# Kernel optimization log

Measured on AMD Instinct MI355X. Metric: run time of the kernel, lower is better.

Reference implementation:

```python
import jax, jax.numpy as jnp
import numpy as np

D_MODEL = 1024
D_STATE = 16
D_CONV = 4
EXPAND = 2
D_INNER = EXPAND * D_MODEL          # 2048
DT_RANK = (D_MODEL + 15) // 16      # 64
B, L = 4, 2048


def setup_inputs() -> dict:
    key = jax.random.key(0)
    ks = jax.random.split(key, 10)
    s = 0.02
    x = jax.random.normal(ks[0], (B, L, D_MODEL), dtype=jnp.float32)
    # weights stored (in, out) so y = x @ W
    W_in = jax.random.normal(ks[1], (D_MODEL, 2 * D_INNER), dtype=jnp.float32) * s
    conv_w = jax.random.normal(ks[2], (D_INNER, D_CONV), dtype=jnp.float32) * 0.2
    conv_b = jnp.zeros((D_INNER,), dtype=jnp.float32)
    W_xproj = jax.random.normal(ks[3], (D_INNER, DT_RANK + 2 * D_STATE), dtype=jnp.float32) * s
    W_dt = jax.random.normal(ks[4], (DT_RANK, D_INNER), dtype=jnp.float32) * s
    b_dt = jax.random.uniform(ks[5], (D_INNER,), dtype=jnp.float32, minval=-4.0, maxval=-2.0)
    # S4D real init: A = -exp(A_log), A_log = log(1..d_state)
    A_log = jnp.log(jnp.broadcast_to(jnp.arange(1, D_STATE + 1, dtype=jnp.float32), (D_INNER, D_STATE)))
    Dp = jnp.ones((D_INNER,), dtype=jnp.float32)
    W_out = jax.random.normal(ks[6], (D_INNER, D_MODEL), dtype=jnp.float32) * s
    return {"x": x, "W_in": W_in, "conv_w": conv_w, "conv_b": conv_b,
            "W_xproj": W_xproj, "W_dt": W_dt, "b_dt": b_dt,
            "A_log": A_log, "Dp": Dp, "W_out": W_out}


def _causal_depthwise_conv(u, conv_w, conv_b):
    # u: (B, L, D_INNER); depthwise causal conv, kernel D_CONV
    uc = jnp.transpose(u, (0, 2, 1))                      # (B, D, L)
    k = conv_w[:, None, :]                                # (D, 1, K)
    y = jax.lax.conv_general_dilated(
        uc, k, window_strides=(1,), padding=[(D_CONV - 1, 0)],
        feature_group_count=D_INNER,
        dimension_numbers=('NCH', 'OIH', 'NCH'))
    y = y + conv_b[None, :, None]
    return jnp.transpose(y, (0, 2, 1))                    # (B, L, D)


def _selective_scan(u, delta, A, Bm, Cm, Dp):
    # u, delta: (B, L, d); A: (d, n); Bm, Cm: (B, L, n)
    def step(h, inp):
        u_t, dt_t, B_t, C_t = inp                         # (B,d),(B,d),(B,n),(B,n)
        dA = jnp.exp(dt_t[..., None] * A)                 # (B, d, n)
        h = h * dA + (dt_t * u_t)[..., None] * B_t[:, None, :]
        y = jnp.einsum('bdn,bn->bd', h, C_t)
        return h, y

    h0 = jnp.zeros((u.shape[0], u.shape[2], A.shape[1]), dtype=u.dtype)
    xs = (jnp.swapaxes(u, 0, 1), jnp.swapaxes(delta, 0, 1),
          jnp.swapaxes(Bm, 0, 1), jnp.swapaxes(Cm, 0, 1))
    _, ys = jax.lax.scan(step, h0, xs)
    y = jnp.swapaxes(ys, 0, 1)                            # (B, L, d)
    return y + u * Dp


def reference(x, W_in, conv_w, conv_b, W_xproj, W_dt, b_dt, A_log, Dp, W_out):
    xz = x @ W_in                                         # (B, L, 2*D_INNER)
    u, z = jnp.split(xz, 2, axis=-1)
    u = jax.nn.silu(_causal_depthwise_conv(u, conv_w, conv_b))
    proj = u @ W_xproj                                    # (B, L, DT_RANK + 2*D_STATE)
    dt_r = proj[..., :DT_RANK]
    Bm = proj[..., DT_RANK:DT_RANK + D_STATE]
    Cm = proj[..., DT_RANK + D_STATE:]
    delta = jax.nn.softplus(dt_r @ W_dt + b_dt)           # (B, L, D_INNER)
    A = -jnp.exp(A_log)                                   # (D_INNER, D_STATE)
    y = _selective_scan(u, delta, A, Bm, Cm, Dp)
    y = y * jax.nn.silu(z)
    return y @ W_out
```

## Files before the change

### kernel.cpp

```cpp
#include <hip/hip_runtime.h>
#include <hip/hip_bf16.h>
#include <math.h>

#define MTOK   8192
#define LSEQ   2048
#define NBATCH 4
#define DMODEL 1024
#define DINNER 2048
#define DSTATE 16
#define DTRANK 64
#define NXZ    4096
#define CHUNK  64
#define NCH    32
#define NPROJ  (MTOK * 96)
#define SPLITK 4

typedef _Float16 f16;
using f16x8 = __attribute__((ext_vector_type(8))) _Float16;
using f16x4 = __attribute__((ext_vector_type(4))) _Float16;
using f32x4 = __attribute__((ext_vector_type(4))) float;

__device__ __forceinline__ float silu_f(float x) { return x / (1.f + __expf(-x)); }

__device__ __forceinline__ void gload_lds16(const void* g, void* l) {
    __builtin_amdgcn_global_load_lds(
        (const __attribute__((address_space(1))) void*)g,
        (__attribute__((address_space(3))) void*)l, 16, 0, 0);
}

__global__ __launch_bounds__(256)
void cvt_f2h(const float* __restrict__ in, f16* __restrict__ out, int n4)
{
    const int i = blockIdx.x * 256 + threadIdx.x;
    if (i >= n4) return;
    const float4 v = ((const float4*)in)[i];
    f16x4 o;
    o[0] = (f16)v.x; o[1] = (f16)v.y; o[2] = (f16)v.z; o[3] = (f16)v.w;
    ((f16x4*)out)[i] = o;
}

__global__ __launch_bounds__(256)
void tcvt(const float* __restrict__ in, f16* __restrict__ out, int R, int C)
{
    __shared__ float t[32][33];
    const int c0 = blockIdx.x * 32, r0 = blockIdx.y * 32;
    const int tx = threadIdx.x & 31, ty = threadIdx.x >> 5;
    #pragma unroll
    for (int j = 0; j < 4; ++j)
        t[ty + 8 * j][tx] = in[(size_t)(r0 + ty + 8 * j) * C + c0 + tx];
    __syncthreads();
    #pragma unroll
    for (int j = 0; j < 4; ++j)
        out[(size_t)(c0 + ty + 8 * j) * R + r0 + tx] = (f16)t[tx][ty + 8 * j];
}

__global__ __launch_bounds__(512, 1)
void hgemm256p(const f16* __restrict__ A, int lda,
               const f16* __restrict__ Bt, int ldb,
               f16* __restrict__ C, int ldc,
               int K, f16* __restrict__ C2, int splitcol)
{
    __shared__ __align__(16) f16 SA[2][16384];
    __shared__ __align__(16) f16 SB[2][16384];

    const int tid  = threadIdx.x;
    const int lane = tid & 63, w = tid >> 6;
    const int wr = w >> 2, wc = w & 3;
    const int row0 = blockIdx.x * 256;
    int col0 = blockIdx.y * 256;

    const int frow = lane & 15;
    const int nt = K / 64;

    auto issue_half = [&](int q) {
        const int t = q >> 2, j = q & 3, buf = t & 1, k0 = t * 64;
        const bool isA = (j >= 2);
        const int hh = j & 1;
        const f16* base = isA ? (A  + (size_t)(row0 + hh * 128) * lda + k0)
                              : (Bt + (size_t)(col0 + hh * 128) * ldb + k0);
        const int ld = isA ? lda : ldb;
        f16* dst = (isA ? &SA[buf][0] : &SB[buf][0]) + hh * 8192;
        #pragma unroll
        for (int r2 = 0; r2 < 2; ++r2) {
            const int ch = r2 * 512 + tid;
            const int grow  = ch >> 3;
            const int gunit = (ch & 7) ^ (grow & 7);
            gload_lds16(base + (size_t)grow * ld + gunit * 8, dst + ch * 8);
        }
    };

    int next = 0;
    for (; next < 6 && next < 4 * nt; ++next) issue_half(next);
    asm volatile("s_waitcnt vmcnt(4)" ::: "memory");
    asm volatile("s_barrier" ::: "memory");

    f32x4 acc[8][4] = {};

    for (int t = 0; t < nt; ++t) {
        const int buf = t & 1;
        const char* Ab = (const char*)&SA[buf][0];
        const char* Bb = (const char*)&SB[buf][0];
        f16x8 bf[4][2];
        #pragma unroll
        for (int p = 0; p < 4; ++p) {
            f16x8 af[2][2];
            if (p == 0) {
                #pragma unroll
                for (int n = 0; n < 4; ++n)
                    #pragma unroll
                    for (int ks = 0; ks < 2; ++ks) {
                        const int R = wc * 64 + n * 16 + frow;
                        const int off = R * 128 +
                            ((ks * 64 + (lane >> 4) * 16) ^ ((R & 7) << 4));
                        bf[n][ks] = *(const f16x8*)(Bb + off);
                    }
            }
            #pragma unroll
            for (int i = 0; i < 2; ++i)
                #pragma unroll
                for (int ks = 0; ks < 2; ++ks) {
                    const int R = wr * 128 + (2 * p + i) * 16 + frow;
                    const int off = R * 128 +
                        ((ks * 64 + (lane >> 4) * 16) ^ ((R & 7) << 4));
                    af[i][ks] = *(const f16x8*)(Ab + off);
                }
            if (next < 4 * nt) issue_half(next++);
            asm volatile("s_barrier" ::: "memory");
            asm volatile("s_waitcnt lgkmcnt(0)" ::: "memory");
            __builtin_amdgcn_sched_barrier(0);
            __builtin_amdgcn_s_setprio(1);
            #pragma unroll
            for (int i = 0; i < 2; ++i)
                #pragma unroll
                for (int n = 0; n < 4; ++n)
                    #pragma unroll
                    for (int ks = 0; ks < 2; ++ks)
                        acc[2 * p + i][n] = __builtin_amdgcn_mfma_f32_16x16x32_f16(
                            af[i][ks], bf[n][ks], acc[2 * p + i][n], 0, 0, 0);
            __builtin_amdgcn_s_setprio(0);
            if (p == 3 && t + 1 < nt) {
                if (next >= 4 * t + 10) asm volatile("s_waitcnt vmcnt(4)" ::: "memory");
                else                    asm volatile("s_waitcnt vmcnt(0)" ::: "memory");
            }
            asm volatile("s_barrier" ::: "memory");
        }
    }

    f16* Cw = C;
    if (C2 != nullptr && col0 >= splitcol) { Cw = C2; col0 -= splitcol; }

    const int rbase = row0 + wr * 128 + (lane >> 4) * 4;
    const int cbase = col0 + wc * 64 + (lane & 15);
    #pragma unroll
    for (int m = 0; m < 8; ++m) {
        #pragma unroll
        for (int n = 0; n < 4; ++n) {
            const int col = cbase + n * 16;
            #pragma unroll
            for (int r = 0; r < 4; ++r)
                Cw[(size_t)(rbase + m * 16 + r) * ldc + col] = (f16)acc[m][n][r];
        }
    }
}

template<int EPI, typename OUT_T>
__global__ __launch_bounds__(256)
void hgemm128(const f16* __restrict__ A, int lda,
              const f16* __restrict__ Bt, int ldb,
              OUT_T* __restrict__ C, int ldc,
              int K, const float* __restrict__ bias,
              OUT_T* __restrict__ C2, int splitcol)
{
    __shared__ __align__(16) f16 As[2][128 * 32];
    __shared__ __align__(16) f16 Bs[2][128 * 32];

    const int tid  = threadIdx.x;
    const int lane = tid & 63, wave = tid >> 6;
    const int wr = wave >> 1, wc = wave & 1;
    const int row0 = blockIdx.x * 128;
    int col0 = blockIdx.y * 128;

    const int lrow = lane >> 2;
    const int lcol = ((lane & 3) ^ ((lane >> 3) & 3)) * 8;
    const f16* Agw = A  + (size_t)(row0 + wave * 32 + lrow) * lda + lcol;
    const f16* Bgw = Bt + (size_t)(col0 + wave * 32 + lrow) * ldb + lcol;
    const int ldsbase = (wave * 32) * 32;

    const int frow = lane & 15;
    const int fk   = (((lane >> 4) ^ ((frow >> 1) & 3))) * 8;
    const int nt = K / 32;

    f32x4 acc[4][4] = {};

    #pragma unroll
    for (int r = 0; r < 2; ++r) {
        gload_lds16(Agw + (size_t)r * 16 * lda, &As[0][ldsbase + r * 16 * 32]);
        gload_lds16(Bgw + (size_t)r * 16 * ldb, &Bs[0][ldsbase + r * 16 * 32]);
    }

    int cur = 0;
    for (int kt = 0; kt < nt; ++kt) {
        __syncthreads();
        if (kt + 1 < nt) {
            const int k0 = (kt + 1) * 32;
            #pragma unroll
            for (int r = 0; r < 2; ++r) {
                gload_lds16(Agw + (size_t)r * 16 * lda + k0, &As[cur ^ 1][ldsbase + r * 16 * 32]);
                gload_lds16(Bgw + (size_t)r * 16 * ldb + k0, &Bs[cur ^ 1][ldsbase + r * 16 * 32]);
            }
        }
        f16x8 af[4], bf[4];
        #pragma unroll
        for (int m = 0; m < 4; ++m)
            af[m] = *(const f16x8*)&As[cur][(wr * 64 + m * 16 + frow) * 32 + fk];
        #pragma unroll
        for (int n = 0; n < 4; ++n)
            bf[n] = *(const f16x8*)&Bs[cur][(wc * 64 + n * 16 + frow) * 32 + fk];
        #pragma unroll
        for (int m = 0; m < 4; ++m)
            #pragma unroll
            for (int n = 0; n < 4; ++n)
                acc[m][n] = __builtin_amdgcn_mfma_f32_16x16x32_f16(af[m], bf[n], acc[m][n], 0, 0, 0);
        cur ^= 1;
    }

    OUT_T* Cw = C;
    if (C2 != nullptr && col0 >= splitcol) { Cw = C2; col0 -= splitcol; }

    const int rbase = row0 + wr * 64 + (lane >> 4) * 4;
    const int cbase = col0 + wc * 64 + (lane & 15);
    #pragma unroll
    for (int m = 0; m < 4; ++m) {
        #pragma unroll
        for (int n = 0; n < 4; ++n) {
            const int col = cbase + n * 16;
            #pragma unroll
            for (int r = 0; r < 4; ++r) {
                const int row = rbase + m * 16 + r;
                float tv = acc[m][n][r];
                if (EPI == 1) {
                    tv += bias[col];
                    tv = (tv > 20.f) ? tv : __logf(1.f + __expf(tv));
                }
                Cw[(size_t)row * ldc + col] = (OUT_T)tv;
            }
        }
    }
}

__global__ __launch_bounds__(256)
void hgemm_n96(const f16* __restrict__ A,
               const f16* __restrict__ Bt,
               float* __restrict__ part)
{
    __shared__ __align__(16) f16 As[128][40];
    __shared__ __align__(16) f16 Bs[96][40];

    const int tid = threadIdx.x, lane = tid & 63, wave = tid >> 6;
    const int row0 = blockIdx.x * 128;
    const int sk = blockIdx.y;
    const int kbase = sk * (DINNER / SPLITK);

    const int srow = tid >> 1, skoff = (tid & 1) * 16;
    const f16* Ag = A  + (size_t)(row0 + srow) * DINNER + kbase + skoff;
    const f16* Bg = Bt + (size_t)srow * DINNER + kbase + skoff;

    const int frow = lane & 15, fk = (lane >> 4) * 8;

    f32x4 acc[2][6] = {};

    for (int kk = 0; kk < DINNER / SPLITK; kk += 32) {
        const f16x8 a0 = *(const f16x8*)(Ag + kk);
        const f16x8 a1 = *(const f16x8*)(Ag + kk + 8);
        f16x8 b0 = {}, b1 = {};
        if (tid < 192) { b0 = *(const f16x8*)(Bg + kk); b1 = *(const f16x8*)(Bg + kk + 8); }
        __syncthreads();
        *(f16x8*)&As[srow][skoff]     = a0;
        *(f16x8*)&As[srow][skoff + 8] = a1;
        if (tid < 192) {
            *(f16x8*)&Bs[srow][skoff]     = b0;
            *(f16x8*)&Bs[srow][skoff + 8] = b1;
        }
        __syncthreads();

        f16x8 af[2], bf[6];
        #pragma unroll
        for (int m = 0; m < 2; ++m)
            af[m] = *(const f16x8*)&As[wave * 32 + m * 16 + frow][fk];
        #pragma unroll
        for (int n = 0; n < 6; ++n)
            bf[n] = *(const f16x8*)&Bs[n * 16 + frow][fk];
        #pragma unroll
        for (int m = 0; m < 2; ++m)
            #pragma unroll
            for (int n = 0; n < 6; ++n)
                acc[m][n] = __builtin_amdgcn_mfma_f32_16x16x32_f16(af[m], bf[n], acc[m][n], 0, 0, 0);
    }

    #pragma unroll
    for (int m = 0; m < 2; ++m)
        #pragma unroll
        for (int n = 0; n < 6; ++n) {
            const int col = n * 16 + (lane & 15);
            #pragma unroll
            for (int r = 0; r < 4; ++r) {
                const int row = row0 + wave * 32 + m * 16 + (lane >> 4) * 4 + r;
                part[((size_t)sk * MTOK + row) * 96 + col] = acc[m][n][r];
            }
        }
}

__global__ __launch_bounds__(256)
void reduce3(const float* __restrict__ part, float* __restrict__ proj,
             f16* __restrict__ projh)
{
    const int e = blockIdx.x * 256 + threadIdx.x;
    float s = 0.f;
    #pragma unroll
    for (int i = 0; i < SPLITK; ++i) s += part[(size_t)i * NPROJ + e];
    proj[e]  = s;
    projh[e] = (f16)s;
}

__global__ __launch_bounds__(256)
void conv_silu_kernel(const f16* __restrict__ uph,
                      const float* __restrict__ cw, const float* __restrict__ cb,
                      f16* __restrict__ uh)
{
    const int mt  = blockIdx.x;
    const int ml0 = mt * 8;
    const int l0  = ml0 & (LSEQ - 1);
    const int d   = threadIdx.x * 8;

    float w[8][4];
    #pragma unroll
    for (int c = 0; c < 8; ++c) {
        const float4 wv = *(const float4*)(cw + (size_t)(d + c) * 4);
        w[c][0] = wv.x; w[c][1] = wv.y; w[c][2] = wv.z; w[c][3] = wv.w;
    }
    float bias[8];
    {
        const float4 b0 = *(const float4*)(cb + d);
        const float4 b1 = *(const float4*)(cb + d + 4);
        bias[0] = b0.x; bias[1] = b0.y; bias[2] = b0.z; bias[3] = b0.w;
        bias[4] = b1.x; bias[5] = b1.y; bias[6] = b1.z; bias[7] = b1.w;
    }

    f16x8 r[11];
    if (l0 != 0) {
        #pragma unroll
        for (int i = 0; i < 11; ++i)
            r[i] = *(const f16x8*)(uph + (size_t)(ml0 - 3 + i) * DINNER + d);
    } else {
        r[0] = f16x8{}; r[1] = f16x8{}; r[2] = f16x8{};
        #pragma unroll
        for (int i = 3; i < 11; ++i)
            r[i] = *(const f16x8*)(uph + (size_t)(ml0 - 3 + i) * DINNER + d);
    }

    #pragma unroll
    for (int i = 0; i < 8; ++i) {
        f16x8 o;
        #pragma unroll
        for (int c = 0; c < 8; ++c) {
            float a = bias[c];
            #pragma unroll
            for (int j = 0; j < 4; ++j)
                a = fmaf((float)r[i + j][c], w[c][j], a);
            o[c] = (f16)silu_f(a);
        }
        *(f16x8*)(uh + (size_t)(ml0 + i) * DINNER + d) = o;
    }
}

__device__ __forceinline__ bool load_A(const float* __restrict__ A_log, int d,
                                       float* Av)
{
    #pragma unroll
    for (int n = 0; n < DSTATE; ++n)
        Av[n] = -__expf(A_log[(size_t)d * DSTATE + n]);
    bool p = true;
    #pragma unroll
    for (int n = 1; n < DSTATE; ++n) {
        const float r = Av[n] / Av[0];
        if (fabsf(r - (float)(n + 1)) > 1e-3f) p = false;
    }
    return p;
}

__global__ __launch_bounds__(256)
void scan_pass1(const f16* __restrict__ uh,
                const f16* __restrict__ deltah,
                const float* __restrict__ proj,
                const float* __restrict__ A_log,
                f16* __restrict__ Sbufh, float* __restrict__ sumdt)
{
    const int d = blockIdx.x * 256 + threadIdx.x;
    const int c = blockIdx.y;
    const int b = blockIdx.z;

    float Av[DSTATE];
    const bool pw = load_A(A_log, d, Av);
    const float Av0 = Av[0];

    const float* projb = proj + ((size_t)b * LSEQ + (size_t)c * CHUNK) * 96 + 64;

    float S[DSTATE];
    #pragma unroll
    for (int n = 0; n < DSTATE; ++n) S[n] = 0.f;
    float sdt = 0.f;

    const size_t tok0 = (size_t)b * LSEQ + (size_t)c * CHUNK;
    if (pw) {
        for (int l = 0; l < CHUNK; ++l) {
            const float* pr = projb + (size_t)l * 96;
            const float dt = (float)deltah[(tok0 + l) * DINNER + d];
            const float uu = (float)uh[(tok0 + l) * DINNER + d];
            sdt += dt;
            const float du = dt * uu;
            const float p1 = __expf(dt * Av0);
            const float p2 = p1 * p1;
            const float p3 = p2 * p1;
            const float p4 = p2 * p2;
            float m = 1.f;
            #pragma unroll
            for (int g = 0; g < 4; ++g) {
                const f32x4 bb = *(const f32x4*)(pr + g * 4);
                S[g*4+0] = fmaf(S[g*4+0], m * p1, du * bb[0]);
                S[g*4+1] = fmaf(S[g*4+1], m * p2, du * bb[1]);
                S[g*4+2] = fmaf(S[g*4+2], m * p3, du * bb[2]);
                S[g*4+3] = fmaf(S[g*4+3], m * p4, du * bb[3]);
                m *= p4;
            }
        }
    } else {
        for (int l = 0; l < CHUNK; ++l) {
            const float* pr = projb + (size_t)l * 96;
            const float dt = (float)deltah[(tok0 + l) * DINNER + d];
            const float uu = (float)uh[(tok0 + l) * DINNER + d];
            sdt += dt;
            const float du = dt * uu;
            #pragma unroll
            for (int n = 0; n < DSTATE; ++n)
                S[n] = fmaf(S[n], __expf(dt * Av[n]), du * pr[n]);
        }
    }

    const size_t base = (size_t)b * NCH + c;
    #pragma unroll
    for (int n = 0; n < DSTATE; ++n)
        Sbufh[(base * DSTATE + n) * DINNER + d] = (f16)S[n];
    sumdt[base * DINNER + d] = sdt;
}

__global__ __launch_bounds__(256)
void scan_pass2(const float* __restrict__ A_log,
                const float* __restrict__ sumdt,
                f16* __restrict__ Sbufh)
{
    const int d = blockIdx.x * 64 + (threadIdx.x & 63);
    const int n = blockIdx.y * 4 + (threadIdx.x >> 6);
    const int b = blockIdx.z;

    const float Avn = -__expf(A_log[(size_t)d * DSTATE + n]);

    float h = 0.f;
    for (int c = 0; c < NCH; ++c) {
        const size_t base = (size_t)b * NCH + c;
        const float sdt = sumdt[base * DINNER + d];
        const size_t idx = (base * DSTATE + n) * DINNER + d;
        const float tmp = (float)Sbufh[idx];
        Sbufh[idx] = (f16)h;
        h = fmaf(h, __expf(sdt * Avn), tmp);
    }
}

__global__ __launch_bounds__(256)
void scan_pass3(const f16* __restrict__ uh,
                const f16* __restrict__ deltah,
                const f16* __restrict__ zh,
                const float* __restrict__ proj,
                const float* __restrict__ A_log,
                const float* __restrict__ Dp,
                const f16* __restrict__ Sbufh,
                f16* __restrict__ ygh)
{
    const int d = blockIdx.x * 256 + threadIdx.x;
    const int c = blockIdx.y;
    const int b = blockIdx.z;

    float Av[DSTATE];
    const bool pw = load_A(A_log, d, Av);
    const float Av0 = Av[0];

    float h[DSTATE];
    const size_t base = (size_t)b * NCH + c;
    #pragma unroll
    for (int n = 0; n < DSTATE; ++n)
        h[n] = (float)Sbufh[(base * DSTATE + n) * DINNER + d];

    const float Dval = Dp[d];
    const float* projb = proj + ((size_t)b * LSEQ + (size_t)c * CHUNK) * 96 + 64;

    const size_t tok0 = (size_t)b * LSEQ + (size_t)c * CHUNK;
    for (int l = 0; l < CHUNK; ++l) {
        const float* pr = projb + (size_t)l * 96;
        const size_t tok = tok0 + l;
        const float dt = (float)deltah[tok * DINNER + d];
        const float uu = (float)uh[tok * DINNER + d];
        const float zz = (float)zh[tok * DINNER + d];
        const float du = dt * uu;
        float y = 0.f;
        if (pw) {
            const float p1 = __expf(dt * Av0);
            const float p2 = p1 * p1;
            const float p3 = p2 * p1;
            const float p4 = p2 * p2;
            float m = 1.f;
            #pragma unroll
            for (int g = 0; g < 4; ++g) {
                const f32x4 bb = *(const f32x4*)(pr + g * 4);
                const f32x4 cc = *(const f32x4*)(pr + 16 + g * 4);
                h[g*4+0] = fmaf(h[g*4+0], m * p1, du * bb[0]);
                h[g*4+1] = fmaf(h[g*4+1], m * p2, du * bb[1]);
                h[g*4+2] = fmaf(h[g*4+2], m * p3, du * bb[2]);
                h[g*4+3] = fmaf(h[g*4+3], m * p4, du * bb[3]);
                y = fmaf(h[g*4+0], cc[0], y);
                y = fmaf(h[g*4+1], cc[1], y);
                y = fmaf(h[g*4+2], cc[2], y);
                y = fmaf(h[g*4+3], cc[3], y);
                m *= p4;
            }
        } else {
            #pragma unroll
            for (int n = 0; n < DSTATE; ++n) {
                h[n] = fmaf(h[n], __expf(dt * Av[n]), du * pr[n]);
                y = fmaf(h[n], pr[16 + n], y);
            }
        }
        const float yt = fmaf(uu, Dval, y);
        ygh[tok * DINNER + d] = (f16)(yt * silu_f(zz));
    }
}

extern "C" void kernel_launch(void* const* d_in, const int* in_sizes, int n_in,
                              void* d_out, int out_size, void* d_ws, size_t ws_size,
                              hipStream_t stream)
{
    const float* x     = (const float*)d_in[0];
    const float* W_in  = (const float*)d_in[1];
    const float* cw    = (const float*)d_in[2];
    const float* cb    = (const float*)d_in[3];
    const float* W_xp  = (const float*)d_in[4];
    const float* W_dt  = (const float*)d_in[5];
    const float* b_dt  = (const float*)d_in[6];
    const float* A_log = (const float*)d_in[7];
    const float* Dp    = (const float*)d_in[8];
    const float* W_out = (const float*)d_in[9];
    float* out = (float*)d_out;

    float* updelta = (float*)d_ws;
    f16*   zh      = (f16*)(updelta + (size_t)MTOK * DINNER);
    f16*   uh      = zh + (size_t)MTOK * DINNER;
    float* proj    = (float*)(uh + (size_t)MTOK * DINNER);
    f16*   projh   = (f16*)(proj + NPROJ);
    f16*   Sbufh   = (f16*)(projh + NPROJ);
    float* sumdt   = (float*)(Sbufh + (size_t)NBATCH * NCH * DSTATE * DINNER * 2);
    f16*   WxpT    = (f16*)(sumdt + (size_t)NBATCH * NCH * DINNER);
    f16*   WdtT    = WxpT + (size_t)96 * DINNER;
    f16*   WoutT   = WdtT + (size_t)DINNER * DTRANK;
    f16*   big     = WoutT + (size_t)DMODEL * DINNER;
    f16*   WinT    = big;
    float* part3   = (float*)(big + (size_t)NXZ * DMODEL);
    f16*   ygh     = big;
    f16*   xh      = uh;
    f16*   uph     = (f16*)updelta;
    f16*   deltah  = (f16*)updelta;

    cvt_f2h<<<(MTOK * DMODEL / 4 + 255) / 256, 256, 0, stream>>>(x, xh, MTOK * DMODEL / 4);
    tcvt<<<dim3(NXZ / 32, DMODEL / 32), 256, 0, stream>>>(W_in, WinT, DMODEL, NXZ);

    hgemm256p<<<dim3(32, 16), 512, 0, stream>>>(
        xh, DMODEL, WinT, DMODEL, uph, DINNER, DMODEL, zh, DINNER);

    conv_silu_kernel<<<MTOK / 8, 256, 0, stream>>>(uph, cw, cb, uh);

    tcvt<<<dim3(96 / 32, DINNER / 32), 256, 0, stream>>>(W_xp, WxpT, DINNER, 96);
    hgemm_n96<<<dim3(64, SPLITK), 256, 0, stream>>>(uh, WxpT, part3);
    reduce3<<<NPROJ / 256, 256, 0, stream>>>(part3, proj, projh);

    tcvt<<<dim3(DINNER / 32, DTRANK / 32), 256, 0, stream>>>(W_dt, WdtT, DTRANK, DINNER);
    hgemm128<1, f16><<<dim3(64, 16), 256, 0, stream>>>(
        projh, 96, WdtT, DTRANK, deltah, DINNER, DTRANK, b_dt, nullptr, 0);

    scan_pass1<<<dim3(DINNER / 256, NCH, NBATCH), 256, 0, stream>>>(
        uh, deltah, proj, A_log, Sbufh, sumdt);
    scan_pass2<<<dim3(DINNER / 64, DSTATE / 4, NBATCH), 256, 0, stream>>>(
        A_log, sumdt, Sbufh);
    scan_pass3<<<dim3(DINNER / 256, NCH, NBATCH), 256, 0, stream>>>(
        uh, deltah, zh, proj, A_log, Dp, Sbufh, ygh);

    tcvt<<<dim3(DMODEL / 32, DINNER / 32), 256, 0, stream>>>(W_out, WoutT, DINNER, DMODEL);
    hgemm128<0, float><<<dim3(64, 8), 256, 0, stream>>>(
        ygh, DINNER, WoutT, DINNER, out, DMODEL, DINNER, nullptr, nullptr, 0);
}
```

Baseline: 296.9 us.

## Fuse delta projection GEMM with scan pass1 and batch weight transposes

Folds the softplus delta GEMM and the first chunked-scan pass into one kernel. Each block computes a 128x128 delta tile with MFMA, stages it in LDS with a swizzle, and runs the per-chunk state accumulation directly from LDS. This avoids re-reading delta from global memory in pass1 and removes one launch. The three small weight transpose launches are also merged into a single kernel issued up front. In exchange, each block does serial GEMM-then-scan work with higher LDS use, and delta is still written out for pass3.

```diff
diff --git a/kernel.cpp b/kernel.cpp
--- a/kernel.cpp
+++ b/kernel.cpp
@@ -39,11 +39,12 @@
     ((f16x4*)out)[i] = o;
 }
 
-__global__ __launch_bounds__(256)
-void tcvt(const float* __restrict__ in, f16* __restrict__ out, int R, int C)
+__device__ __forceinline__ void tcvt_body(const float* __restrict__ in,
+                                          f16* __restrict__ out,
+                                          int R, int C, int bx, int by)
 {
     __shared__ float t[32][33];
-    const int c0 = blockIdx.x * 32, r0 = blockIdx.y * 32;
+    const int c0 = bx * 32, r0 = by * 32;
     const int tx = threadIdx.x & 31, ty = threadIdx.x >> 5;
     #pragma unroll
     for (int j = 0; j < 4; ++j)
@@ -52,6 +53,29 @@
     #pragma unroll
     for (int j = 0; j < 4; ++j)
         out[(size_t)(c0 + ty + 8 * j) * R + r0 + tx] = (f16)t[tx][ty + 8 * j];
+}
+
+__global__ __launch_bounds__(256)
+void tcvt(const float* __restrict__ in, f16* __restrict__ out, int R, int C)
+{
+    tcvt_body(in, out, R, C, blockIdx.x, blockIdx.y);
+}
+
+__global__ __launch_bounds__(256)
+void tcvt3(const float* __restrict__ W_xp, f16* __restrict__ WxpT,
+           const float* __restrict__ W_dt, f16* __restrict__ WdtT,
+           const float* __restrict__ W_out, f16* __restrict__ WoutT)
+{
+    int id = blockIdx.x;
+    if (id < 192) {
+        tcvt_body(W_xp, WxpT, DINNER, 96, id % 3, id / 3);
+    } else if (id < 320) {
+        id -= 192;
+        tcvt_body(W_dt, WdtT, DTRANK, DINNER, id % 64, id / 64);
+    } else {
+        id -= 320;
+        tcvt_body(W_out, WoutT, DINNER, DMODEL, id % 32, id / 32);
+    }
 }
 
 __global__ __launch_bounds__(512, 1)
@@ -249,6 +273,155 @@
 }
 
 __global__ __launch_bounds__(256)
+void delta_scan1(const f16* __restrict__ A,
+                 const f16* __restrict__ Bt,
+                 f16* __restrict__ deltah,
+                 const float* __restrict__ bias,
+                 const f16* __restrict__ uh,
+                 const float* __restrict__ proj,
+                 const float* __restrict__ A_log,
+                 f16* __restrict__ Sbufh, float* __restrict__ sumdt)
+{
+    __shared__ __align__(16) f16 smem[16384];
+    __shared__ float Bsh[128][16];
+    f16* As = smem;
+    f16* Bs = smem + 8192;
+
+    const int tid  = threadIdx.x;
+    const int lane = tid & 63, wave = tid >> 6;
+    const int wr = wave >> 1, wc = wave & 1;
+    const int row0 = blockIdx.x * 128;
+    const int col0 = blockIdx.y * 128;
+
+    const int lrow = lane >> 2;
+    const int lcol = ((lane & 3) ^ ((lane >> 3) & 3)) * 8;
+    const f16* Agw = A  + (size_t)(row0 + wave * 32 + lrow) * 96 + lcol;
+    const f16* Bgw = Bt + (size_t)(col0 + wave * 32 + lrow) * 64 + lcol;
+    const int ldsbase = (wave * 32) * 32;
+
+    const int frow = lane & 15;
+    const int fk   = (((lane >> 4) ^ ((frow >> 1) & 3))) * 8;
+
+    f32x4 acc[4][4] = {};
+
+    #pragma unroll
+    for (int r = 0; r < 2; ++r) {
+        gload_lds16(Agw + (size_t)r * 16 * 96, &As[ldsbase + r * 16 * 32]);
+        gload_lds16(Bgw + (size_t)r * 16 * 64, &Bs[ldsbase + r * 16 * 32]);
+    }
+
+    int cur = 0;
+    #pragma unroll
+    for (int kt = 0; kt < 2; ++kt) {
+        __syncthreads();
+        if (kt == 0) {
+            #pragma unroll
+            for (int r = 0; r < 2; ++r) {
+                gload_lds16(Agw + (size_t)r * 16 * 96 + 32, &As[4096 + ldsbase + r * 16 * 32]);
+                gload_lds16(Bgw + (size_t)r * 16 * 64 + 32, &Bs[4096 + ldsbase + r * 16 * 32]);
+            }
+        }
+        f16x8 af[4], bf[4];
+        #pragma unroll
+        for (int m = 0; m < 4; ++m)
+            af[m] = *(const f16x8*)&As[cur * 4096 + (wr * 64 + m * 16 + frow) * 32 + fk];
+        #pragma unroll
+        for (int n = 0; n < 4; ++n)
+            bf[n] = *(const f16x8*)&Bs[cur * 4096 + (wc * 64 + n * 16 + frow) * 32 + fk];
+        #pragma unroll
+        for (int m = 0; m < 4; ++m)
+            #pragma unroll
+            for (int n = 0; n < 4; ++n)
+                acc[m][n] = __builtin_amdgcn_mfma_f32_16x16x32_f16(af[m], bf[n], acc[m][n], 0, 0, 0);
+        cur ^= 1;
+    }
+
+    __syncthreads();
+    f16* dlt = smem;
+
+    const int rloc0 = wr * 64 + (lane >> 4) * 4;
+    const int cloc0 = wc * 64 + (lane & 15);
+    #pragma unroll
+    for (int m = 0; m < 4; ++m) {
+        #pragma unroll
+        for (int n = 0; n < 4; ++n) {
+            const int cl = cloc0 + n * 16;
+            #pragma unroll
+            for (int r = 0; r < 4; ++r) {
+                const int rl = rloc0 + m * 16 + r;
+                float tv = acc[m][n][r] + bias[col0 + cl];
+                tv = (tv > 20.f) ? tv : __logf(1.f + __expf(tv));
+                const f16 hv = (f16)tv;
+                deltah[(size_t)(row0 + rl) * DINNER + col0 + cl] = hv;
+                dlt[rl * 128 + (cl ^ (((rl >> 2) & 3) << 4))] = hv;
+            }
+        }
+    }
+
+    #pragma unroll
+    for (int i = 0; i < 8; ++i) {
+        const int f = i * 256 + tid;
+        Bsh[f >> 4][f & 15] = proj[(size_t)(row0 + (f >> 4)) * 96 + 64 + (f & 15)];
+    }
+    __syncthreads();
+
+    const int cl2 = tid >> 7, dl = tid & 127;
+    const int d = col0 + dl;
+    const int b = row0 >> 11;
+    const int cb = ((row0 & (LSEQ - 1)) >> 6) + cl2;
+    const size_t tok0 = (size_t)row0 + cl2 * 64;
+
+    float Av[DSTATE];
+    #pragma unroll
+    for (int n = 0; n < DSTATE; ++n)
+        Av[n] = -__expf(A_log[(size_t)d * DSTATE + n]);
+    bool pw = true;
+    #pragma unroll
+    for (int n = 1; n < DSTATE; ++n)
+        if (fabsf(Av[n] / Av[0] - (float)(n + 1)) > 1e-3f) pw = false;
+    const float Av0 = Av[0];
+
+    float S[DSTATE];
+    #pragma unroll
+    for (int n = 0; n < DSTATE; ++n) S[n] = 0.f;
+    float sdt = 0.f;
+
+    for (int l = 0; l < CHUNK; ++l) {
+        const int rl = cl2 * 64 + l;
+        const float dt = (float)dlt[rl * 128 + (dl ^ (((rl >> 2) & 3) << 4))];
+        const float uu = (float)uh[(tok0 + l) * DINNER + d];
+        sdt += dt;
+        const float du = dt * uu;
+        if (pw) {
+            const float p1 = __expf(dt * Av0);
+            const float p2 = p1 * p1;
+            const float p3 = p2 * p1;
+            const float p4 = p2 * p2;
+            float mm = 1.f;
+            #pragma unroll
+            for (int g = 0; g < 4; ++g) {
+                const f32x4 bb = *(const f32x4*)&Bsh[rl][g * 4];
+                S[g*4+0] = fmaf(S[g*4+0], mm * p1, du * bb[0]);
+                S[g*4+1] = fmaf(S[g*4+1], mm * p2, du * bb[1]);
+                S[g*4+2] = fmaf(S[g*4+2], mm * p3, du * bb[2]);
+                S[g*4+3] = fmaf(S[g*4+3], mm * p4, du * bb[3]);
+                mm *= p4;
+            }
+        } else {
+            #pragma unroll
+            for (int n = 0; n < DSTATE; ++n)
+                S[n] = fmaf(S[n], __expf(dt * Av[n]), du * Bsh[rl][n]);
+        }
+    }
+
+    const size_t base = (size_t)b * NCH + cb;
+    #pragma unroll
+    for (int n = 0; n < DSTATE; ++n)
+        Sbufh[(base * DSTATE + n) * DINNER + d] = (f16)S[n];
+    sumdt[base * DINNER + d] = sdt;
+}
+
+__global__ __launch_bounds__(256)
 void hgemm_n96(const f16* __restrict__ A,
                const f16* __restrict__ Bt,
                float* __restrict__ part)
@@ -386,71 +559,6 @@
         if (fabsf(r - (float)(n + 1)) > 1e-3f) p = false;
     }
     return p;
-}
-
-__global__ __launch_bounds__(256)
-void scan_pass1(const f16* __restrict__ uh,
-                const f16* __restrict__ deltah,
-                const float* __restrict__ proj,
-                const float* __restrict__ A_log,
-                f16* __restrict__ Sbufh, float* __restrict__ sumdt)
-{
-    const int d = blockIdx.x * 256 + threadIdx.x;
-    const int c = blockIdx.y;
-    const int b = blockIdx.z;
-
-    float Av[DSTATE];
-    const bool pw = load_A(A_log, d, Av);
-    const float Av0 = Av[0];
-
-    const float* projb = proj + ((size_t)b * LSEQ + (size_t)c * CHUNK) * 96 + 64;
-
-    float S[DSTATE];
-    #pragma unroll
-    for (int n = 0; n < DSTATE; ++n) S[n] = 0.f;
-    float sdt = 0.f;
-
-    const size_t tok0 = (size_t)b * LSEQ + (size_t)c * CHUNK;
-    if (pw) {
-        for (int l = 0; l < CHUNK; ++l) {
-            const float* pr = projb + (size_t)l * 96;
-            const float dt = (float)deltah[(tok0 + l) * DINNER + d];
-            const float uu = (float)uh[(tok0 + l) * DINNER + d];
-            sdt += dt;
-            const float du = dt * uu;
-            const float p1 = __expf(dt * Av0);
-            const float p2 = p1 * p1;
-            const float p3 = p2 * p1;
-            const float p4 = p2 * p2;
-            float m = 1.f;
-            #pragma unroll
-            for (int g = 0; g < 4; ++g) {
-                const f32x4 bb = *(const f32x4*)(pr + g * 4);
-                S[g*4+0] = fmaf(S[g*4+0], m * p1, du * bb[0]);
-                S[g*4+1] = fmaf(S[g*4+1], m * p2, du * bb[1]);
-                S[g*4+2] = fmaf(S[g*4+2], m * p3, du * bb[2]);
-                S[g*4+3] = fmaf(S[g*4+3], m * p4, du * bb[3]);
-                m *= p4;
-            }
-        }
-    } else {
-        for (int l = 0; l < CHUNK; ++l) {
-            const float* pr = projb + (size_t)l * 96;
-            const float dt = (float)deltah[(tok0 + l) * DINNER + d];
-            const float uu = (float)uh[(tok0 + l) * DINNER + d];
-            sdt += dt;
-            const float du = dt * uu;
-            #pragma unroll
-            for (int n = 0; n < DSTATE; ++n)
-                S[n] = fmaf(S[n], __expf(dt * Av[n]), du * pr[n]);
-        }
-    }
-
-    const size_t base = (size_t)b * NCH + c;
-    #pragma unroll
-    for (int n = 0; n < DSTATE; ++n)
-        Sbufh[(base * DSTATE + n) * DINNER + d] = (f16)S[n];
-    sumdt[base * DINNER + d] = sdt;
 }
 
 __global__ __launch_bounds__(256)
@@ -579,28 +687,24 @@
 
     cvt_f2h<<<(MTOK * DMODEL / 4 + 255) / 256, 256, 0, stream>>>(x, xh, MTOK * DMODEL / 4);
     tcvt<<<dim3(NXZ / 32, DMODEL / 32), 256, 0, stream>>>(W_in, WinT, DMODEL, NXZ);
+    tcvt3<<<2368, 256, 0, stream>>>(W_xp, WxpT, W_dt, WdtT, W_out, WoutT);
 
     hgemm256p<<<dim3(32, 16), 512, 0, stream>>>(
         xh, DMODEL, WinT, DMODEL, uph, DINNER, DMODEL, zh, DINNER);
 
     conv_silu_kernel<<<MTOK / 8, 256, 0, stream>>>(uph, cw, cb, uh);
 
-    tcvt<<<dim3(96 / 32, DINNER / 32), 256, 0, stream>>>(W_xp, WxpT, DINNER, 96);
     hgemm_n96<<<dim3(64, SPLITK), 256, 0, stream>>>(uh, WxpT, part3);
     reduce3<<<NPROJ / 256, 256, 0, stream>>>(part3, proj, projh);
 
-    tcvt<<<dim3(DINNER / 32, DTRANK / 32), 256, 0, stream>>>(W_dt, WdtT, DTRANK, DINNER);
-    hgemm128<1, f16><<<dim3(64, 16), 256, 0, stream>>>(
-        projh, 96, WdtT, DTRANK, deltah, DINNER, DTRANK, b_dt, nullptr, 0);
-
-    scan_pass1<<<dim3(DINNER / 256, NCH, NBATCH), 256, 0, stream>>>(
-        uh, deltah, proj, A_log, Sbufh, sumdt);
+    delta_scan1<<<dim3(64, 16), 256, 0, stream>>>(
+        projh, WdtT, deltah, b_dt, uh, proj, A_log, Sbufh, sumdt);
+
     scan_pass2<<<dim3(DINNER / 64, DSTATE / 4, NBATCH), 256, 0, stream>>>(
         A_log, sumdt, Sbufh);
     scan_pass3<<<dim3(DINNER / 256, NCH, NBATCH), 256, 0, stream>>>(
         uh, deltah, zh, proj, A_log, Dp, Sbufh, ygh);
 
-    tcvt<<<dim3(DMODEL / 32, DINNER / 32), 256, 0, stream>>>(W_out, WoutT, DINNER, DMODEL);
     hgemm128<0, float><<<dim3(64, 8), 256, 0, stream>>>(
         ygh, DINNER, WoutT, DINNER, out, DMODEL, DINNER, nullptr, nullptr, 0);
 }
```

Result: slower. 313.2 us (+5.5%).
